# Optimization experiments

Hardware: AMD Instinct MI355X
Metric: run time of the kernel (lower is better)

## Reference

```python
import jax, jax.numpy as jnp
import numpy as np

D_MODEL = 1024
NUM_HEADS = 16
HEAD_DIM = D_MODEL // NUM_HEADS  # 64
N = 1024
B = 8


def setup_inputs() -> dict:
    key = jax.random.key(0)
    ks = jax.random.split(key, 11)
    s = 0.02
    inp = {
        'query': jax.random.normal(ks[0], (B, D_MODEL, N), jnp.float32),
        'key':   jax.random.normal(ks[1], (B, D_MODEL, N), jnp.float32),
        'value': jax.random.normal(ks[2], (B, D_MODEL, N), jnp.float32),
        # 1x1 conv1d == linear over channel dim: weight [out, in], bias [out]
        'Wq': jax.random.normal(ks[3], (D_MODEL, D_MODEL), jnp.float32) * s,
        'bq': jax.random.normal(ks[4], (D_MODEL,), jnp.float32) * s,
        'Wk': jax.random.normal(ks[5], (D_MODEL, D_MODEL), jnp.float32) * s,
        'bk': jax.random.normal(ks[6], (D_MODEL,), jnp.float32) * s,
        'Wv': jax.random.normal(ks[7], (D_MODEL, D_MODEL), jnp.float32) * s,
        'bv': jax.random.normal(ks[8], (D_MODEL,), jnp.float32) * s,
        'Wm': jax.random.normal(ks[9], (D_MODEL, D_MODEL), jnp.float32) * s,
        'bm': jax.random.normal(ks[10], (D_MODEL,), jnp.float32) * s,
    }
    return inp


def _proj(W, b, x):
    # nn.Conv1d(kernel_size=1): out[b,o,n] = sum_i W[o,i] x[b,i,n] + b[o]
    return jnp.einsum('oi,bin->bon', W, x) + b[None, :, None]


def reference(query, key, value, Wq, bq, Wk, bk, Wv, bv, Wm, bm):
    Bd = query.shape[0]
    # view(B, dim, heads, N): channel axis split as (head_dim, num_heads)
    q = _proj(Wq, bq, query).reshape(Bd, HEAD_DIM, NUM_HEADS, -1)
    k = _proj(Wk, bk, key).reshape(Bd, HEAD_DIM, NUM_HEADS, -1)
    v = _proj(Wv, bv, value).reshape(Bd, HEAD_DIM, NUM_HEADS, -1)
    scale = 1.0 / (HEAD_DIM ** 0.5)
    scores = jnp.einsum('bdhn,bdhm->bhnm', q, k) * scale  # [B,H,N,N]
    prob = jax.nn.softmax(scores, axis=-1)
    x = jnp.einsum('bhnm,bdhm->bdhn', prob, v)  # [B,D,H,N]
    out = _proj(Wm, bm, x.reshape(Bd, HEAD_DIM * NUM_HEADS, -1))
    return out
```

## Files before the change

kernel.cpp:

```cpp
#include <hip/hip_runtime.h>

typedef __bf16 bf16x8 __attribute__((ext_vector_type(8)));
typedef __bf16 bf16x4 __attribute__((ext_vector_type(4)));
typedef float f32x4 __attribute__((ext_vector_type(4)));
typedef unsigned short u16;
typedef unsigned int u32;

typedef union { bf16x8 v8; bf16x4 v4[2]; } bfu;

__device__ __forceinline__ u16 f2bf(float f) {
  u32 u = __builtin_bit_cast(u32, f);
  u = (u + 0x7FFFu + ((u >> 16) & 1u)) >> 16;
  return (u16)u;
}

__device__ __forceinline__ void gload_lds16(const void* g, void* l) {
  __builtin_amdgcn_global_load_lds((const __attribute__((address_space(1))) void*)g,
                                   (__attribute__((address_space(3))) void*)l, 16, 0, 0);
}

__global__ __launch_bounds__(256) void transpose_cast3(const float* __restrict__ q,
                                                       const float* __restrict__ k,
                                                       const float* __restrict__ v,
                                                       u16* __restrict__ X3) {
  __shared__ float T[64][68];
  int tid = threadIdx.x;
  int n0 = blockIdx.x * 64, i0 = blockIdx.y * 64;
  int z = blockIdx.z;
  int which = z >> 3, b = z & 7;
  const float* src = (which == 0) ? q : (which == 1) ? k : v;
  size_t boff = (size_t)b << 20;
  const float* s = src + boff;
  u16* d = X3 + ((size_t)which << 23) + boff;
  int ir = tid >> 4, n4 = (tid & 15) * 4;
#pragma unroll
  for (int r = 0; r < 4; ++r) {
    int i_loc = ir + r * 16;
    float4 vv = *(const float4*)(s + (size_t)(i0 + i_loc) * 1024 + n0 + n4);
    *(float4*)&T[i_loc][n4] = vv;
  }
  __syncthreads();
  int nr = tid >> 3, i8 = (tid & 7) * 8;
#pragma unroll
  for (int r = 0; r < 2; ++r) {
    int n_loc = nr + r * 32;
    u32 pk[4];
#pragma unroll
    for (int j = 0; j < 4; ++j) {
      float f0 = T[i8 + 2 * j][n_loc];
      float f1 = T[i8 + 2 * j + 1][n_loc];
      pk[j] = (u32)f2bf(f0) | ((u32)f2bf(f1) << 16);
    }
    *(uint4*)(d + (size_t)(n0 + n_loc) * 1024 + i0 + i8) = make_uint4(pk[0], pk[1], pk[2], pk[3]);
  }
}

__global__ __launch_bounds__(256) void transpose_cast(const float* __restrict__ src,
                                                      u16* __restrict__ dst) {
  __shared__ float T[64][68];
  int tid = threadIdx.x;
  int n0 = blockIdx.x * 64, i0 = blockIdx.y * 64;
  size_t boff = (size_t)blockIdx.z << 20;
  const float* s = src + boff;
  u16* d = dst + boff;
  int ir = tid >> 4, n4 = (tid & 15) * 4;
#pragma unroll
  for (int r = 0; r < 4; ++r) {
    int i_loc = ir + r * 16;
    float4 v = *(const float4*)(s + (size_t)(i0 + i_loc) * 1024 + n0 + n4);
    *(float4*)&T[i_loc][n4] = v;
  }
  __syncthreads();
  int nr = tid >> 3, i8 = (tid & 7) * 8;
#pragma unroll
  for (int r = 0; r < 2; ++r) {
    int n_loc = nr + r * 32;
    u32 pk[4];
#pragma unroll
    for (int j = 0; j < 4; ++j) {
      float f0 = T[i8 + 2 * j][n_loc];
      float f1 = T[i8 + 2 * j + 1][n_loc];
      pk[j] = (u32)f2bf(f0) | ((u32)f2bf(f1) << 16);
    }
    *(uint4*)(d + (size_t)(n0 + n_loc) * 1024 + i0 + i8) = make_uint4(pk[0], pk[1], pk[2], pk[3]);
  }
}

__global__ __launch_bounds__(256) void cast_weights(const float* __restrict__ Wq,
                                                    const float* __restrict__ Wk,
                                                    const float* __restrict__ Wv,
                                                    const float* __restrict__ Wm,
                                                    u16* __restrict__ out) {
  int w = blockIdx.y;
  const float* src = (w == 0) ? Wq : (w == 1) ? Wk : (w == 2) ? Wv : Wm;
  u16* dst = out + ((size_t)w << 20);
  int o = blockIdx.x;
  int c4 = threadIdx.x * 4;
  float f[4];
  if (w < 3) {
    float4 v = *(const float4*)(src + (size_t)o * 1024 + c4);
    f[0] = v.x; f[1] = v.y; f[2] = v.z; f[3] = v.w;
  } else {
#pragma unroll
    for (int j = 0; j < 4; ++j) {
      int cp = c4 + j;
      f[j] = src[(size_t)o * 1024 + (cp & 63) * 16 + (cp >> 6)];
    }
  }
  u32 p0 = (u32)f2bf(f[0]) | ((u32)f2bf(f[1]) << 16);
  u32 p1 = (u32)f2bf(f[2]) | ((u32)f2bf(f[3]) << 16);
  *(uint2*)(dst + (size_t)o * 1024 + c4) = make_uint2(p0, p1);
}

__device__ __forceinline__ void gemm_body(const u16* __restrict__ A,
                                          const u16* __restrict__ B,
                                          const float* __restrict__ bias,
                                          void* __restrict__ Out, float escale,
                                          int epi, u16* LD) {
  int tid = threadIdx.x;
  int wave = tid >> 6, l = tid & 63, ln = l & 15, g = l >> 4;
  int wm = wave >> 2, wn = wave & 3;
  int bid = blockIdx.x;
  int mt = (bid >> 3) & 7;
  int nt = ((bid & 7) << 2) | (bid >> 6);
  int c0 = mt * 128, n0 = nt * 256;

  int R = tid >> 3, sl = tid & 7;
  int v = sl ^ (R & 7);
  int sa = v >> 2, sg = v & 3;
  const u16* aSrc = A + (size_t)(c0 + 2 * R + sa) * 1024 + sg * 8;
  const u16* bSrc0 = B + (size_t)(n0 + 2 * R + sa) * 1024 + sg * 8;
  const u16* bSrc1 = B + (size_t)(n0 + 128 + 2 * R + sa) * 1024 + sg * 8;

  int slr = ((((ln & 1) << 2) | g) ^ ((ln >> 1) & 7)) * 8;
  int laneA = (wm * 32 + (ln >> 1)) * 64 + slr;
  int laneB = (wn * 32 + (ln >> 1)) * 64 + slr;

  f32x4 acc[4][4] = {};

#define STAGE(buf, kt)                                                   \
  do {                                                                   \
    gload_lds16(aSrc + (kt) * 32, &LD[(buf) * 4096 + tid * 8]);          \
    gload_lds16(bSrc0 + (kt) * 32, &LD[16384 + (buf) * 8192 + tid * 8]); \
    gload_lds16(bSrc1 + (kt) * 32,                                       \
                &LD[16384 + (buf) * 8192 + 4096 + tid * 8]);             \
  } while (0)

  STAGE(0, 0);
  STAGE(1, 1);
  STAGE(2, 2);

#pragma unroll
  for (int t = 0; t < 32; ++t) {
    if (t < 30)
      asm volatile("s_waitcnt vmcnt(6)" ::: "memory");
    else if (t == 30)
      asm volatile("s_waitcnt vmcnt(3)" ::: "memory");
    else
      asm volatile("s_waitcnt vmcnt(0)" ::: "memory");
    asm volatile("s_barrier" ::: "memory");
    if (t <= 28) STAGE((t + 3) & 3, t + 3);
    const int ab = (t & 3) * 4096;
    const int bb = 16384 + (t & 3) * 8192;
    bf16x8 af[4], bfr[4];
#pragma unroll
    for (int mm = 0; mm < 4; ++mm) af[mm] = *(const bf16x8*)&LD[ab + laneA + mm * 512];
#pragma unroll
    for (int nn = 0; nn < 4; ++nn) bfr[nn] = *(const bf16x8*)&LD[bb + laneB + nn * 512];
    __builtin_amdgcn_s_setprio(1);
#pragma unroll
    for (int mm = 0; mm < 4; ++mm)
#pragma unroll
      for (int nn = 0; nn < 4; ++nn)
        acc[mm][nn] = __builtin_amdgcn_mfma_f32_16x16x32_bf16(af[mm], bfr[nn], acc[mm][nn], 0, 0, 0);
    __builtin_amdgcn_s_setprio(0);
  }
#undef STAGE

  int D0 = (c0 >> 4) + wm * 4;
#pragma unroll
  for (int nn = 0; nn < 4; ++nn) {
    size_t ng = (size_t)n0 + wn * 64 + nn * 16 + ln;
#pragma unroll
    for (int r = 0; r < 4; ++r) {
      int h = g * 4 + r;
      if (epi == 0) {
        bf16x4 pk;
#pragma unroll
        for (int mm = 0; mm < 4; ++mm) {
          int c = c0 + wm * 64 + mm * 16 + h;
          pk[mm] = (__bf16)((acc[mm][nn][r] + bias[c]) * escale);
        }
        *(bf16x4*)((u16*)Out + ng * 1024 + (size_t)h * 64 + D0) = pk;
      } else {
        size_t b = ng >> 10, n = ng & 1023;
#pragma unroll
        for (int mm = 0; mm < 4; ++mm) {
          int c = c0 + wm * 64 + mm * 16 + h;
          float val = (acc[mm][nn][r] + bias[c]) * escale;
          if (epi == 1) {
            int d = D0 + mm;
            ((u16*)Out)[((b * 16 + h) * 64 + d) * 1024 + n] = f2bf(val);
          } else {
            ((float*)Out)[(b << 20) + (size_t)c * 1024 + n] = val;
          }
        }
      }
    }
  }
}

template <int EPI>
__global__ __launch_bounds__(512, 2) void gemm4b(const u16* __restrict__ A,
                                                 const u16* __restrict__ B,
                                                 const float* __restrict__ bias,
                                                 void* __restrict__ Out, float escale) {
  __shared__ u16 LD[49152];
  gemm_body(A, B, bias, Out, escale, EPI, LD);
}

__global__ __launch_bounds__(512, 2) void gemm_qkv(const u16* __restrict__ Wbf,
                                                   const u16* __restrict__ X3,
                                                   const float* __restrict__ bq,
                                                   const float* __restrict__ bk,
                                                   const float* __restrict__ bv,
                                                   u16* __restrict__ Qh,
                                                   u16* __restrict__ Kh,
                                                   u16* __restrict__ Vt, float qscale) {
  __shared__ u16 LD[49152];
  int z = blockIdx.y;
  const u16* A = Wbf + ((size_t)z << 20);
  const u16* B = X3 + ((size_t)z << 23);
  const float* bias = (z == 0) ? bq : (z == 1) ? bk : bv;
  void* Out = (z == 0) ? (void*)Qh : (z == 1) ? (void*)Kh : (void*)Vt;
  float escale = (z == 0) ? qscale : 1.0f;
  int epi = (z == 2) ? 1 : 0;
  gemm_body(A, B, bias, Out, escale, epi, LD);
}

__global__ __launch_bounds__(256, 2) void attn_kernel(const u16* __restrict__ Qh,
                                                      const u16* __restrict__ Kh,
                                                      const u16* __restrict__ Vt,
                                                      u16* __restrict__ Xh) {
  __shared__ u16 Ks[2][4096];
  __shared__ u16 Vs[2][4096];
  int tid = threadIdx.x;
  int w = tid >> 6, l = tid & 63, ln = l & 15, g = l >> 4;
  int id = blockIdx.x;
  int bh7 = id & 7;
  int qp = (id >> 3) & 3;
  int bh = (id >> 5) * 8 + bh7;
  size_t b = bh >> 4;
  int h = bh & 15;
  const u16* Qg = Qh + (b << 20) + (h << 6);
  const u16* Kg = Kh + (b << 20) + (h << 6);
  const u16* Vg = Vt + ((size_t)bh << 16);
  u16* Og = Xh + (b << 20) + (h << 6);

  bf16x8 qf[4][2];
#pragma unroll
  for (int t = 0; t < 4; ++t)
#pragma unroll
    for (int kk = 0; kk < 2; ++kk)
      qf[t][kk] = *(const bf16x8*)(Qg + (size_t)(qp * 256 + t * 64 + w * 16 + ln) * 1024 + kk * 32 + g * 8);

  int lr = l >> 3;
  int sw8 = ((l & 7) ^ lr) << 3;
  int r0 = w * 16 + lr, r1 = r0 + 8;
  const u16* kS0 = Kg + (size_t)r0 * 1024 + sw8;
  const u16* kS1 = Kg + (size_t)r1 * 1024 + sw8;
  const u16* vS0 = Vg + (size_t)r0 * 1024 + sw8;
  const u16* vS1 = Vg + (size_t)r1 * 1024 + sw8;

  f32x4 xacc[4][4] = {};
  float lacc[4] = {0.f, 0.f, 0.f, 0.f};

  gload_lds16(kS0, &Ks[0][(w * 2) * 512]);
  gload_lds16(kS1, &Ks[0][(w * 2 + 1) * 512]);
  gload_lds16(vS0, &Vs[0][(w * 2) * 512]);
  gload_lds16(vS1, &Vs[0][(w * 2 + 1) * 512]);
  __syncthreads();

  int sx = ln & 7;
  int cur = 0;
  for (int kt = 0; kt < 16; ++kt) {
    if (kt < 15) {
      int nxt = cur ^ 1;
      gload_lds16(kS0 + (size_t)(kt + 1) * 65536, &Ks[nxt][(w * 2) * 512]);
      gload_lds16(kS1 + (size_t)(kt + 1) * 65536, &Ks[nxt][(w * 2 + 1) * 512]);
      gload_lds16(vS0 + (kt + 1) * 64, &Vs[nxt][(w * 2) * 512]);
      gload_lds16(vS1 + (kt + 1) * 64, &Vs[nxt][(w * 2 + 1) * 512]);
    }
    bf16x8 kf[2][4];
#pragma unroll
    for (int kk = 0; kk < 2; ++kk)
#pragma unroll
      for (int f = 0; f < 4; ++f) {
        int slot = (((kk << 2) + g) ^ sx) << 3;
        kf[kk][f] = *(const bf16x8*)&Ks[cur][(f * 16 + ln) * 64 + slot];
      }
    bf16x8 vf[2][4];
#pragma unroll
    for (int kk = 0; kk < 2; ++kk) {
      int s0 = (kk << 2) + (g >> 1);
      int off = (g & 1) << 2;
#pragma unroll
      for (int fd = 0; fd < 4; ++fd) {
        int rowb = (fd * 16 + ln) * 64;
        bfu uv;
        uv.v4[0] = *(const bf16x4*)&Vs[cur][rowb + ((s0 ^ sx) << 3) + off];
        uv.v4[1] = *(const bf16x4*)&Vs[cur][rowb + (((s0 + 2) ^ sx) << 3) + off];
        vf[kk][fd] = uv.v8;
      }
    }
#pragma unroll
    for (int t = 0; t < 4; ++t) {
      f32x4 sacc[4] = {};
#pragma unroll
      for (int kk = 0; kk < 2; ++kk)
#pragma unroll
        for (int f = 0; f < 4; ++f)
          sacc[f] = __builtin_amdgcn_mfma_f32_16x16x32_bf16(kf[kk][f], qf[t][kk], sacc[f], 0, 0, 0);
      bf16x8 pf[2];
#pragma unroll
      for (int kk = 0; kk < 2; ++kk) {
        bfu up;
#pragma unroll
        for (int e2 = 0; e2 < 2; ++e2) {
          int f = 2 * kk + e2;
          float p0 = __builtin_amdgcn_exp2f(sacc[f][0]);
          float p1 = __builtin_amdgcn_exp2f(sacc[f][1]);
          float p2 = __builtin_amdgcn_exp2f(sacc[f][2]);
          float p3 = __builtin_amdgcn_exp2f(sacc[f][3]);
          lacc[t] += (p0 + p1) + (p2 + p3);
          bf16x4 pb;
          pb[0] = (__bf16)p0; pb[1] = (__bf16)p1; pb[2] = (__bf16)p2; pb[3] = (__bf16)p3;
          up.v4[e2] = pb;
        }
        pf[kk] = up.v8;
      }
#pragma unroll
      for (int kk = 0; kk < 2; ++kk)
#pragma unroll
        for (int fd = 0; fd < 4; ++fd)
          xacc[t][fd] = __builtin_amdgcn_mfma_f32_16x16x32_bf16(pf[kk], vf[kk][fd], xacc[t][fd], 0, 0, 0);
    }
    __syncthreads();
    cur ^= 1;
  }

#pragma unroll
  for (int t = 0; t < 4; ++t) {
    float lt = lacc[t];
    lt += __shfl_xor(lt, 16);
    lt += __shfl_xor(lt, 32);
    float il[4];
#pragma unroll
    for (int r = 0; r < 4; ++r) il[r] = 1.0f / __shfl(lt, g * 4 + r);
#pragma unroll
    for (int fd = 0; fd < 4; ++fd)
#pragma unroll
      for (int r = 0; r < 4; ++r) {
        int nq = qp * 256 + t * 64 + w * 16 + g * 4 + r;
        Og[(size_t)nq * 1024 + fd * 16 + ln] = f2bf(xacc[t][fd][r] * il[r]);
      }
  }
}

extern "C" void kernel_launch(void* const* d_in, const int* in_sizes, int n_in,
                              void* d_out, int out_size, void* d_ws, size_t ws_size,
                              hipStream_t stream) {
  const float* q  = (const float*)d_in[0];
  const float* k  = (const float*)d_in[1];
  const float* v  = (const float*)d_in[2];
  const float* Wq = (const float*)d_in[3];
  const float* bq = (const float*)d_in[4];
  const float* Wk = (const float*)d_in[5];
  const float* bk = (const float*)d_in[6];
  const float* Wv = (const float*)d_in[7];
  const float* bv = (const float*)d_in[8];
  const float* Wm = (const float*)d_in[9];
  const float* bm = (const float*)d_in[10];

  char* ws = (char*)d_ws;
  u16* Wbf = (u16*)ws;
  u16* Qh  = (u16*)(ws + (8ull << 20));
  u16* Kh  = (u16*)(ws + (24ull << 20));
  u16* Vt  = (u16*)(ws + (40ull << 20));
  u16* X3  = (u16*)(ws + (56ull << 20));

  cast_weights<<<dim3(1024, 4, 1), 256, 0, stream>>>(Wq, Wk, Wv, Wm, Wbf);

  const float qscale = 0.125f * 1.44269504088896340736f;

  if (ws_size >= (104ull << 20)) {
    transpose_cast3<<<dim3(16, 16, 24), 256, 0, stream>>>(q, k, v, X3);
    gemm_qkv<<<dim3(256, 3), 512, 0, stream>>>(Wbf, X3, bq, bk, bv, Qh, Kh, Vt, qscale);
  } else {
    dim3 tg(16, 16, 8);
    transpose_cast<<<tg, 256, 0, stream>>>(q, X3);
    gemm4b<0><<<256, 512, 0, stream>>>(Wbf, X3, bq, Qh, qscale);
    transpose_cast<<<tg, 256, 0, stream>>>(k, X3);
    gemm4b<0><<<256, 512, 0, stream>>>(Wbf + (1u << 20), X3, bk, Kh, 1.0f);
    transpose_cast<<<tg, 256, 0, stream>>>(v, X3);
    gemm4b<1><<<256, 512, 0, stream>>>(Wbf + (2u << 20), X3, bv, Vt, 1.0f);
  }

  attn_kernel<<<512, 256, 0, stream>>>(Qh, Kh, Vt, X3);

  gemm4b<2><<<256, 512, 0, stream>>>(Wbf + (3u << 20), X3, bm, d_out, 1.0f);
}
```

Before: 170.9 us.

## Use 4-wave GEMM blocks with larger per-wave tiles and triple-buffered LDS

The projection GEMMs move from 512-thread blocks (8 waves, 32x64 output per wave) to 256-thread blocks (4 waves, 64x128 output per wave). Each wave now keeps 32 accumulator tiles instead of 16, which improves LDS operand reuse per MFMA, and each thread issues six global-to-LDS loads per stage. The LDS pipeline drops from four buffers to three, prefetching two stages ahead instead of three, which cuts shared memory per block. The trade-offs are higher register pressure, fewer waves per CU to hide latency, and a shallower prefetch.

New measurement: 171.9 us. No clear change (+0.6%).

```diff
diff --git a/kernel.cpp b/kernel.cpp
--- a/kernel.cpp
+++ b/kernel.cpp
@@ -119,68 +119,68 @@
                                           int epi, u16* LD) {
   int tid = threadIdx.x;
   int wave = tid >> 6, l = tid & 63, ln = l & 15, g = l >> 4;
-  int wm = wave >> 2, wn = wave & 3;
+  int wm = wave >> 1, wn = wave & 1;
   int bid = blockIdx.x;
   int mt = (bid >> 3) & 7;
   int nt = ((bid & 7) << 2) | (bid >> 6);
   int c0 = mt * 128, n0 = nt * 256;
 
-  int R = tid >> 3, sl = tid & 7;
-  int v = sl ^ (R & 7);
-  int sa = v >> 2, sg = v & 3;
-  const u16* aSrc = A + (size_t)(c0 + 2 * R + sa) * 1024 + sg * 8;
-  const u16* bSrc0 = B + (size_t)(n0 + 2 * R + sa) * 1024 + sg * 8;
-  const u16* bSrc1 = B + (size_t)(n0 + 128 + 2 * R + sa) * 1024 + sg * 8;
+  int R = tid >> 3;
+  int v = (tid & 7) ^ (R & 7);
+  const u16* aS = A + (size_t)(c0 + 2 * R + (v >> 2)) * 1024 + (v & 3) * 8;
+  const u16* bS = B + (size_t)(n0 + 2 * R + (v >> 2)) * 1024 + (v & 3) * 8;
 
   int slr = ((((ln & 1) << 2) | g) ^ ((ln >> 1) & 7)) * 8;
   int laneA = (wm * 32 + (ln >> 1)) * 64 + slr;
-  int laneB = (wn * 32 + (ln >> 1)) * 64 + slr;
-
-  f32x4 acc[4][4] = {};
-
-#define STAGE(buf, kt)                                                   \
-  do {                                                                   \
-    gload_lds16(aSrc + (kt) * 32, &LD[(buf) * 4096 + tid * 8]);          \
-    gload_lds16(bSrc0 + (kt) * 32, &LD[16384 + (buf) * 8192 + tid * 8]); \
-    gload_lds16(bSrc1 + (kt) * 32,                                       \
-                &LD[16384 + (buf) * 8192 + 4096 + tid * 8]);             \
+  int laneB = (wn * 64 + (ln >> 1)) * 64 + slr;
+
+  f32x4 acc[4][8] = {};
+
+#define STAGE(buf, kt)                                                        \
+  do {                                                                        \
+    gload_lds16(aS + (kt) * 32, &LD[(buf) * 4096 + tid * 8]);                 \
+    gload_lds16(aS + 65536 + (kt) * 32, &LD[(buf) * 4096 + 2048 + tid * 8]);  \
+    gload_lds16(bS + (kt) * 32, &LD[12288 + (buf) * 8192 + tid * 8]);         \
+    gload_lds16(bS + 65536 + (kt) * 32,                                       \
+                &LD[12288 + (buf) * 8192 + 2048 + tid * 8]);                  \
+    gload_lds16(bS + 131072 + (kt) * 32,                                      \
+                &LD[12288 + (buf) * 8192 + 4096 + tid * 8]);                  \
+    gload_lds16(bS + 196608 + (kt) * 32,                                      \
+                &LD[12288 + (buf) * 8192 + 6144 + tid * 8]);                  \
   } while (0)
 
   STAGE(0, 0);
   STAGE(1, 1);
-  STAGE(2, 2);
 
 #pragma unroll
   for (int t = 0; t < 32; ++t) {
-    if (t < 30)
+    if (t < 31)
       asm volatile("s_waitcnt vmcnt(6)" ::: "memory");
-    else if (t == 30)
-      asm volatile("s_waitcnt vmcnt(3)" ::: "memory");
     else
       asm volatile("s_waitcnt vmcnt(0)" ::: "memory");
     asm volatile("s_barrier" ::: "memory");
-    if (t <= 28) STAGE((t + 3) & 3, t + 3);
-    const int ab = (t & 3) * 4096;
-    const int bb = 16384 + (t & 3) * 8192;
-    bf16x8 af[4], bfr[4];
+    if (t <= 29) STAGE((t + 2) % 3, t + 2);
+    const int ab = (t % 3) * 4096;
+    const int bb = 12288 + (t % 3) * 8192;
+    bf16x8 af[4];
 #pragma unroll
     for (int mm = 0; mm < 4; ++mm) af[mm] = *(const bf16x8*)&LD[ab + laneA + mm * 512];
-#pragma unroll
-    for (int nn = 0; nn < 4; ++nn) bfr[nn] = *(const bf16x8*)&LD[bb + laneB + nn * 512];
     __builtin_amdgcn_s_setprio(1);
 #pragma unroll
-    for (int mm = 0; mm < 4; ++mm)
-#pragma unroll
-      for (int nn = 0; nn < 4; ++nn)
-        acc[mm][nn] = __builtin_amdgcn_mfma_f32_16x16x32_bf16(af[mm], bfr[nn], acc[mm][nn], 0, 0, 0);
+    for (int nn = 0; nn < 8; ++nn) {
+      bf16x8 bfr = *(const bf16x8*)&LD[bb + laneB + nn * 512];
+#pragma unroll
+      for (int mm = 0; mm < 4; ++mm)
+        acc[mm][nn] = __builtin_amdgcn_mfma_f32_16x16x32_bf16(af[mm], bfr, acc[mm][nn], 0, 0, 0);
+    }
     __builtin_amdgcn_s_setprio(0);
   }
 #undef STAGE
 
   int D0 = (c0 >> 4) + wm * 4;
 #pragma unroll
-  for (int nn = 0; nn < 4; ++nn) {
-    size_t ng = (size_t)n0 + wn * 64 + nn * 16 + ln;
+  for (int nn = 0; nn < 8; ++nn) {
+    size_t ng = (size_t)n0 + wn * 128 + nn * 16 + ln;
 #pragma unroll
     for (int r = 0; r < 4; ++r) {
       int h = g * 4 + r;
@@ -211,15 +211,15 @@
 }
 
 template <int EPI>
-__global__ __launch_bounds__(512, 2) void gemm4b(const u16* __restrict__ A,
+__global__ __launch_bounds__(256, 2) void gemm4b(const u16* __restrict__ A,
                                                  const u16* __restrict__ B,
                                                  const float* __restrict__ bias,
                                                  void* __restrict__ Out, float escale) {
-  __shared__ u16 LD[49152];
+  __shared__ u16 LD[36864];
   gemm_body(A, B, bias, Out, escale, EPI, LD);
 }
 
-__global__ __launch_bounds__(512, 2) void gemm_qkv(const u16* __restrict__ Wbf,
+__global__ __launch_bounds__(256, 2) void gemm_qkv(const u16* __restrict__ Wbf,
                                                    const u16* __restrict__ X3,
                                                    const float* __restrict__ bq,
                                                    const float* __restrict__ bk,
@@ -227,7 +227,7 @@
                                                    u16* __restrict__ Qh,
                                                    u16* __restrict__ Kh,
                                                    u16* __restrict__ Vt, float qscale) {
-  __shared__ u16 LD[49152];
+  __shared__ u16 LD[36864];
   int z = blockIdx.y;
   const u16* A = Wbf + ((size_t)z << 20);
   const u16* B = X3 + ((size_t)z << 23);
@@ -395,18 +395,18 @@
 
   if (ws_size >= (104ull << 20)) {
     transpose_cast3<<<dim3(16, 16, 24), 256, 0, stream>>>(q, k, v, X3);
-    gemm_qkv<<<dim3(256, 3), 512, 0, stream>>>(Wbf, X3, bq, bk, bv, Qh, Kh, Vt, qscale);
+    gemm_qkv<<<dim3(256, 3), 256, 0, stream>>>(Wbf, X3, bq, bk, bv, Qh, Kh, Vt, qscale);
   } else {
     dim3 tg(16, 16, 8);
     transpose_cast<<<tg, 256, 0, stream>>>(q, X3);
-    gemm4b<0><<<256, 512, 0, stream>>>(Wbf, X3, bq, Qh, qscale);
+    gemm4b<0><<<256, 256, 0, stream>>>(Wbf, X3, bq, Qh, qscale);
     transpose_cast<<<tg, 256, 0, stream>>>(k, X3);
-    gemm4b<0><<<256, 512, 0, stream>>>(Wbf + (1u << 20), X3, bk, Kh, 1.0f);
+    gemm4b<0><<<256, 256, 0, stream>>>(Wbf + (1u << 20), X3, bk, Kh, 1.0f);
     transpose_cast<<<tg, 256, 0, stream>>>(v, X3);
-    gemm4b<1><<<256, 512, 0, stream>>>(Wbf + (2u << 20), X3, bv, Vt, 1.0f);
+    gemm4b<1><<<256, 256, 0, stream>>>(Wbf + (2u << 20), X3, bv, Vt, 1.0f);
   }
 
   attn_kernel<<<512, 256, 0, stream>>>(Qh, Kh, Vt, X3);
 
-  gemm4b<2><<<256, 512, 0, stream>>>(Wbf + (3u << 20), X3, bm, d_out, 1.0f);
-}
+  gemm4b<2><<<256, 256, 0, stream>>>(Wbf + (3u << 20), X3, bm, d_out, 1.0f);
+}
```
